# Kernel tuning notes

Measured on AMD Instinct MI355X. Metric: run time of the kernel, lower is better.

Reference implementation:

```python
import jax, jax.numpy as jnp
import numpy as np
import math

N_QUBITS = 6
N_LAYERS = 3
OUT_DIM = 8
B = 131072
F = 24


def _gate_rx(a):
    # RX(a) = [[cos(a/2), -i sin(a/2)], [-i sin(a/2), cos(a/2)]]; a: scalar or [B]
    c = jnp.cos(a / 2).astype(jnp.complex64)
    s = (-1j * jnp.sin(a / 2)).astype(jnp.complex64)
    return jnp.stack([jnp.stack([c, s], -1), jnp.stack([s, c], -1)], -2)


def _gate_ry(a):
    c = jnp.cos(a / 2).astype(jnp.complex64)
    s = jnp.sin(a / 2).astype(jnp.complex64)
    return jnp.stack([jnp.stack([c, -s], -1), jnp.stack([s, c], -1)], -2)


def _gate_rz(a):
    # RZ(a) = diag(e^{-ia/2}, e^{ia/2})
    e = jnp.exp(-0.5j * a.astype(jnp.complex64))
    z = jnp.zeros_like(e)
    return jnp.stack([jnp.stack([e, z], -1), jnp.stack([z, jnp.conj(e)], -1)], -2)


def _apply_1q(state, gate, q, batched):
    # state: [B] + [2]*N_QUBITS ; gate: [2,2] or [B,2,2]
    s = jnp.moveaxis(state, 1 + q, 1)
    if batched:
        out = jnp.einsum('bij,bj...->bi...', gate, s)
    else:
        out = jnp.einsum('ij,bj...->bi...', gate, s)
    return jnp.moveaxis(out, 1, 1 + q)


def _apply_cnot(state, c, t):
    # flip target where control bit == 1
    cax = 1 + c
    s0 = jnp.take(state, 0, axis=cax)
    s1 = jnp.take(state, 1, axis=cax)
    tax = 1 + t if t < c else t  # control axis removed
    s1 = jnp.flip(s1, axis=tax)
    return jnp.stack([s0, s1], axis=cax)


def _circuit(x, theta):
    Bn = x.shape[0]
    # pooling branch of forward: chunks of size ceil(F/n_qubits)=4, mean each
    x_packed = x.reshape(Bn, N_QUBITS, F // N_QUBITS).mean(-1)
    angles = jnp.clip(x_packed, -6.0, 6.0) / 6.0 * math.pi  # [B, n_qubits]

    state = jnp.zeros((Bn,) + (2,) * N_QUBITS, dtype=jnp.complex64)
    state = state.at[(slice(None),) + (0,) * N_QUBITS].set(1.0)

    # angle encoding: RX(a_q), RZ(0.5*a_q) per qubit (batched gates)
    for q in range(N_QUBITS):
        state = _apply_1q(state, _gate_rx(angles[:, q]), q, batched=True)
        state = _apply_1q(state, _gate_rz(0.5 * angles[:, q]), q, batched=True)

    for l in range(N_LAYERS):
        for q in range(N_QUBITS - 1):
            state = _apply_cnot(state, q, q + 1)
        state = _apply_cnot(state, N_QUBITS - 1, 0)
        for q in range(N_QUBITS):
            state = _apply_1q(state, _gate_rx(theta[l, q, 0]), q, batched=False)
            state = _apply_1q(state, _gate_ry(theta[l, q, 1]), q, batched=False)
            state = _apply_1q(state, _gate_rz(theta[l, q, 2]), q, batched=False)

    probs = jnp.abs(state) ** 2  # real
    meas = []
    for k in range(OUT_DIM):
        q = k % N_QUBITS
        if k % 2 == 0:  # PauliZ
            pq = jnp.sum(probs, axis=tuple(a for a in range(1, N_QUBITS + 1) if a != 1 + q))
            meas.append(pq[:, 0] - pq[:, 1])
        else:  # PauliX: Re <psi| X_q |psi>
            flipped = jnp.flip(state, axis=1 + q)
            meas.append(jnp.real(jnp.sum(jnp.conj(state) * flipped, axis=tuple(range(1, N_QUBITS + 1)))))
    return jnp.stack(meas, axis=1).astype(jnp.float32)  # [B, out_dim]


def setup_inputs() -> dict:
    key = jax.random.key(0)
    k1, k2 = jax.random.split(key)
    x = jax.random.normal(k1, (B, F), dtype=jnp.float32)
    theta = jax.random.normal(k2, (N_LAYERS, N_QUBITS, 3), dtype=jnp.float32) * 0.1
    return {"x": x, "theta": theta}


def reference(x, theta):
    return _circuit(x, theta)
```

## Files before the change

### kernel.cpp

```cpp
#include <hip/hip_runtime.h>
#include <math.h>


struct cf { float r, i; };

__device__ __forceinline__ cf cmul(cf a, cf b) {
    return { fmaf(a.r, b.r, -a.i * b.i), fmaf(a.r, b.i, a.i * b.r) };
}
__device__ __forceinline__ cf cmac(cf acc, cf g, cf v) {
    acc.r = fmaf(g.r, v.r, fmaf(-g.i, v.i, acc.r));
    acc.i = fmaf(g.r, v.i, fmaf(g.i, v.r, acc.i));
    return acc;
}

template<int M>
__device__ __forceinline__ void apply1q(cf* st, cf g00, cf g01, cf g10, cf g11) {
#pragma unroll
    for (int i = 0; i < 64; ++i) {
        if (i & M) continue;
        cf a = st[i], b = st[i + M];
        cf na = cmul(g00, a); na = cmac(na, g01, b);
        cf nb = cmul(g10, a); nb = cmac(nb, g11, b);
        st[i] = na; st[i + M] = nb;
    }
}

template<int MC, int MT>
__device__ __forceinline__ void cnot(cf* st) {
#pragma unroll
    for (int i = 0; i < 64; ++i) {
        if ((i & MC) && !(i & MT)) {
            cf tmp = st[i]; st[i] = st[i + MT]; st[i + MT] = tmp;
        }
    }
}

__global__ __launch_bounds__(256, 2) void qsim_kernel(
    const float* __restrict__ x, const float* __restrict__ theta,
    float* __restrict__ out) {
    __shared__ float gs[18 * 8];
    const int t = threadIdx.x;
    if (t < 18) {
        const float* th = theta + t * 3;
        float sx, cx, sy, cy, sz, cz;
        __sincosf(0.5f * th[0], &sx, &cx);
        __sincosf(0.5f * th[1], &sy, &cy);
        __sincosf(0.5f * th[2], &sz, &cz);
        cf m00 = {  cy * cx,  sy * sx };
        cf m01 = { -sy * cx, -cy * sx };
        cf m10 = {  sy * cx, -cy * sx };
        cf m11 = {  cy * cx, -sy * sx };
        cf e0 = { cz, -sz }, e1 = { cz, sz };
        cf g00 = cmul(e0, m00), g01 = cmul(e0, m01);
        cf g10 = cmul(e1, m10), g11 = cmul(e1, m11);
        float* o = gs + t * 8;
        o[0] = g00.r; o[1] = g00.i; o[2] = g01.r; o[3] = g01.i;
        o[4] = g10.r; o[5] = g10.i; o[6] = g11.r; o[7] = g11.i;
    }
    __syncthreads();

    const int b = blockIdx.x * 256 + t;

    const float4* xv = reinterpret_cast<const float4*>(x + (size_t)b * 24);
    cf v0[6], v1[6];
#pragma unroll
    for (int q = 0; q < 6; ++q) {
        float4 xq = xv[q];
        float m = (xq.x + xq.y + xq.z + xq.w) * 0.25f;
        m = fminf(fmaxf(m, -6.0f), 6.0f);
        float a = m * 0.52359877559829887308f;
        float s2, c2, s4, c4;
        __sincosf(0.50f * a, &s2, &c2);
        __sincosf(0.25f * a, &s4, &c4);
        v0[q] = { c4 * c2, -s4 * c2 };
        v1[q] = { s4 * s2, -c4 * s2 };
    }

    cf st[64];
    st[0] = v0[0]; st[32] = v1[0];
#pragma unroll
    for (int q = 1; q < 6; ++q) {
        const int m = 32 >> q;
#pragma unroll
        for (int i = 0; i < 64; i += 2 * m) {
            st[i + m] = cmul(st[i], v1[q]);
            st[i]     = cmul(st[i], v0[q]);
        }
    }

#pragma unroll
    for (int l = 0; l < 3; ++l) {
        cnot<32, 16>(st);
        cnot<16,  8>(st);
        cnot< 8,  4>(st);
        cnot< 4,  2>(st);
        cnot< 2,  1>(st);
        cnot< 1, 32>(st);
        const float* g = gs + l * 48;
#define G4(o) cf{g[(o)+0], g[(o)+1]}, cf{g[(o)+2], g[(o)+3]}, \
              cf{g[(o)+4], g[(o)+5]}, cf{g[(o)+6], g[(o)+7]}
        apply1q<32>(st, G4(0));
        apply1q<16>(st, G4(8));
        apply1q< 8>(st, G4(16));
        apply1q< 4>(st, G4(24));
        apply1q< 2>(st, G4(32));
        apply1q< 1>(st, G4(40));
#undef G4
    }

    float s[8] = {0, 0, 0, 0, 0, 0, 0, 0};
#pragma unroll
    for (int i = 0; i < 64; ++i) {
        float p = fmaf(st[i].r, st[i].r, st[i].i * st[i].i);
        const int gi = (((i >> 5) & 1) << 2) | (((i >> 3) & 1) << 1) | ((i >> 1) & 1);
        s[gi] += p;
    }
    float z0 = (s[0] + s[1] + s[2] + s[3]) - (s[4] + s[5] + s[6] + s[7]);
    float z2 = (s[0] + s[1] + s[4] + s[5]) - (s[2] + s[3] + s[6] + s[7]);
    float z4 = (s[0] + s[2] + s[4] + s[6]) - (s[1] + s[3] + s[5] + s[7]);

    float x1 = 0.0f, x3 = 0.0f, x5 = 0.0f;
#pragma unroll
    for (int i = 0; i < 64; ++i) {
        if (!(i & 16)) x1 = fmaf(st[i].r, st[i + 16].r, fmaf(st[i].i, st[i + 16].i, x1));
        if (!(i &  4)) x3 = fmaf(st[i].r, st[i +  4].r, fmaf(st[i].i, st[i +  4].i, x3));
        if (!(i &  1)) x5 = fmaf(st[i].r, st[i +  1].r, fmaf(st[i].i, st[i +  1].i, x5));
    }
    x1 *= 2.0f; x3 *= 2.0f; x5 *= 2.0f;

    float4* ov = reinterpret_cast<float4*>(out + (size_t)b * 8);
    ov[0] = make_float4(z0, x1, z2, x3);
    ov[1] = make_float4(z4, x5, z0, x1);
}

extern "C" void kernel_launch(void* const* d_in, const int* in_sizes, int n_in,
                              void* d_out, int out_size, void* d_ws, size_t ws_size,
                              hipStream_t stream) {
    const float* x     = (const float*)d_in[0];
    const float* theta = (const float*)d_in[1];
    float* out = (float*)d_out;
    const int B = in_sizes[0] / 24;
    qsim_kernel<<<dim3(B / 256), dim3(256), 0, stream>>>(x, theta, out);
}
```

Measured before the change: 88.52 us.

## Split each statevector across four lanes using DPP cross-lane exchanges

Each 64-amplitude state is now spread across four lanes with 16 amplitudes per lane, and the launch uses four times as many threads. The two high qubits become lane bits, so their gates, CNOTs and measurements use DPP lane shuffles and selects. Per-thread register use drops, which allows higher occupancy (launch bounds raised to 4 blocks). In exchange, every lane redundantly loads the input and computes its trig, shuffle instructions are added, and outputs become scattered scalar stores.

Result: no change. 89.97 us (+1.6%).

```diff
diff --git a/kernel.cpp b/kernel.cpp
--- a/kernel.cpp
+++ b/kernel.cpp
@@ -13,10 +13,21 @@
     return acc;
 }
 
+constexpr int DPP_X1  = 0xB1;
+constexpr int DPP_X2  = 0x4E;
+constexpr int DPP_C01 = 0xB4;
+
+template<int CTRL>
+__device__ __forceinline__ float dppf(float v) {
+    return __int_as_float(__builtin_amdgcn_mov_dpp(__float_as_int(v), CTRL, 0xF, 0xF, true));
+}
+template<int CTRL>
+__device__ __forceinline__ cf dppc(cf v) { return { dppf<CTRL>(v.r), dppf<CTRL>(v.i) }; }
+
 template<int M>
 __device__ __forceinline__ void apply1q(cf* st, cf g00, cf g01, cf g10, cf g11) {
 #pragma unroll
-    for (int i = 0; i < 64; ++i) {
+    for (int i = 0; i < 16; ++i) {
         if (i & M) continue;
         cf a = st[i], b = st[i + M];
         cf na = cmul(g00, a); na = cmac(na, g01, b);
@@ -25,17 +36,29 @@
     }
 }
 
-template<int MC, int MT>
-__device__ __forceinline__ void cnot(cf* st) {
+template<int XCTRL>
+__device__ __forceinline__ void apply1q_lane(cf* st, bool hi, cf g00, cf g01, cf g10, cf g11) {
+    cf ga, gb;
+    ga.r = hi ? g11.r : g00.r;  ga.i = hi ? g11.i : g00.i;
+    gb.r = hi ? g10.r : g01.r;  gb.i = hi ? g10.i : g01.i;
 #pragma unroll
-    for (int i = 0; i < 64; ++i) {
-        if ((i & MC) && !(i & MT)) {
-            cf tmp = st[i]; st[i] = st[i + MT]; st[i + MT] = tmp;
-        }
+    for (int i = 0; i < 16; ++i) {
+        cf part = dppc<XCTRL>(st[i]);
+        cf n = cmul(ga, st[i]);
+        n = cmac(n, gb, part);
+        st[i] = n;
     }
 }
 
-__global__ __launch_bounds__(256, 2) void qsim_kernel(
+template<int MC, int MT>
+__device__ __forceinline__ void cnot_local(cf* st) {
+#pragma unroll
+    for (int i = 0; i < 16; ++i) {
+        if ((i & MC) && !(i & MT)) { cf t = st[i]; st[i] = st[i + MT]; st[i + MT] = t; }
+    }
+}
+
+__global__ __launch_bounds__(256, 4) void qsim_kernel(
     const float* __restrict__ x, const float* __restrict__ theta,
     float* __restrict__ out) {
     __shared__ float gs[18 * 8];
@@ -59,9 +82,13 @@
     }
     __syncthreads();
 
-    const int b = blockIdx.x * 256 + t;
+    const int g = blockIdx.x * 256 + t;
+    const int e = g >> 2;
+    const int p = g & 3;
+    const bool l1 = (p & 2) != 0;
+    const bool l0 = (p & 1) != 0;
 
-    const float4* xv = reinterpret_cast<const float4*>(x + (size_t)b * 24);
+    const float4* xv = reinterpret_cast<const float4*>(x + (size_t)e * 24);
     cf v0[6], v1[6];
 #pragma unroll
     for (int q = 0; q < 6; ++q) {
@@ -76,61 +103,79 @@
         v1[q] = { s4 * s2, -c4 * s2 };
     }
 
-    cf st[64];
-    st[0] = v0[0]; st[32] = v1[0];
+    cf f0, f1;
+    f0.r = l1 ? v1[0].r : v0[0].r;  f0.i = l1 ? v1[0].i : v0[0].i;
+    f1.r = l0 ? v1[1].r : v0[1].r;  f1.i = l0 ? v1[1].i : v0[1].i;
+
+    cf st[16];
+    st[0] = cmul(f0, f1);
 #pragma unroll
-    for (int q = 1; q < 6; ++q) {
-        const int m = 32 >> q;
+    for (int q = 2; q < 6; ++q) {
+        const int m = 8 >> (q - 2);
 #pragma unroll
-        for (int i = 0; i < 64; i += 2 * m) {
+        for (int i = 0; i < 16; i += 2 * m) {
             st[i + m] = cmul(st[i], v1[q]);
             st[i]     = cmul(st[i], v0[q]);
         }
     }
 
+#pragma unroll 1
+    for (int l = 0; l < 3; ++l) {
 #pragma unroll
-    for (int l = 0; l < 3; ++l) {
-        cnot<32, 16>(st);
-        cnot<16,  8>(st);
-        cnot< 8,  4>(st);
-        cnot< 4,  2>(st);
-        cnot< 2,  1>(st);
-        cnot< 1, 32>(st);
-        const float* g = gs + l * 48;
-#define G4(o) cf{g[(o)+0], g[(o)+1]}, cf{g[(o)+2], g[(o)+3]}, \
-              cf{g[(o)+4], g[(o)+5]}, cf{g[(o)+6], g[(o)+7]}
-        apply1q<32>(st, G4(0));
-        apply1q<16>(st, G4(8));
-        apply1q< 8>(st, G4(16));
-        apply1q< 4>(st, G4(24));
-        apply1q< 2>(st, G4(32));
-        apply1q< 1>(st, G4(40));
+        for (int i = 0; i < 16; ++i) st[i] = dppc<DPP_C01>(st[i]);
+#pragma unroll
+        for (int i = 0; i < 8; ++i) {
+            cf lo = st[i], hi = st[i + 8];
+            st[i].r     = l0 ? hi.r : lo.r;  st[i].i     = l0 ? hi.i : lo.i;
+            st[i + 8].r = l0 ? lo.r : hi.r;  st[i + 8].i = l0 ? lo.i : hi.i;
+        }
+        cnot_local<8, 4>(st);
+        cnot_local<4, 2>(st);
+        cnot_local<2, 1>(st);
+#pragma unroll
+        for (int i = 1; i < 16; i += 2) st[i] = dppc<DPP_X2>(st[i]);
+
+        const float* gg = gs + l * 48;
+#define G4(k) cf{gg[8*(k)+0], gg[8*(k)+1]}, cf{gg[8*(k)+2], gg[8*(k)+3]}, \
+              cf{gg[8*(k)+4], gg[8*(k)+5]}, cf{gg[8*(k)+6], gg[8*(k)+7]}
+        apply1q_lane<DPP_X2>(st, l1, G4(0));
+        apply1q_lane<DPP_X1>(st, l0, G4(1));
+        apply1q<8>(st, G4(2));
+        apply1q<4>(st, G4(3));
+        apply1q<2>(st, G4(4));
+        apply1q<1>(st, G4(5));
 #undef G4
     }
 
-    float s[8] = {0, 0, 0, 0, 0, 0, 0, 0};
+    float z0 = 0.f, z2 = 0.f, z4 = 0.f, x1s = 0.f, x3s = 0.f, x5s = 0.f;
 #pragma unroll
-    for (int i = 0; i < 64; ++i) {
-        float p = fmaf(st[i].r, st[i].r, st[i].i * st[i].i);
-        const int gi = (((i >> 5) & 1) << 2) | (((i >> 3) & 1) << 1) | ((i >> 1) & 1);
-        s[gi] += p;
+    for (int i = 0; i < 16; ++i) {
+        float pr = fmaf(st[i].r, st[i].r, st[i].i * st[i].i);
+        z0 += pr;
+        z2 = (i & 8) ? z2 - pr : z2 + pr;
+        z4 = (i & 2) ? z4 - pr : z4 + pr;
+        cf part = dppc<DPP_X1>(st[i]);
+        x1s = fmaf(st[i].r, part.r, fmaf(st[i].i, part.i, x1s));
     }
-    float z0 = (s[0] + s[1] + s[2] + s[3]) - (s[4] + s[5] + s[6] + s[7]);
-    float z2 = (s[0] + s[1] + s[4] + s[5]) - (s[2] + s[3] + s[6] + s[7]);
-    float z4 = (s[0] + s[2] + s[4] + s[6]) - (s[1] + s[3] + s[5] + s[7]);
+    if (l1) z0 = -z0;
+#pragma unroll
+    for (int i = 0; i < 16; ++i) {
+        if (!(i & 4)) x3s = fmaf(st[i].r, st[i + 4].r, fmaf(st[i].i, st[i + 4].i, x3s));
+        if (!(i & 1)) x5s = fmaf(st[i].r, st[i + 1].r, fmaf(st[i].i, st[i + 1].i, x5s));
+    }
+    x3s *= 2.f; x5s *= 2.f;
 
-    float x1 = 0.0f, x3 = 0.0f, x5 = 0.0f;
-#pragma unroll
-    for (int i = 0; i < 64; ++i) {
-        if (!(i & 16)) x1 = fmaf(st[i].r, st[i + 16].r, fmaf(st[i].i, st[i + 16].i, x1));
-        if (!(i &  4)) x3 = fmaf(st[i].r, st[i +  4].r, fmaf(st[i].i, st[i +  4].i, x3));
-        if (!(i &  1)) x5 = fmaf(st[i].r, st[i +  1].r, fmaf(st[i].i, st[i +  1].i, x5));
-    }
-    x1 *= 2.0f; x3 *= 2.0f; x5 *= 2.0f;
+    z0  += dppf<DPP_X1>(z0);   z0  += dppf<DPP_X2>(z0);
+    z2  += dppf<DPP_X1>(z2);   z2  += dppf<DPP_X2>(z2);
+    z4  += dppf<DPP_X1>(z4);   z4  += dppf<DPP_X2>(z4);
+    x1s += dppf<DPP_X1>(x1s);  x1s += dppf<DPP_X2>(x1s);
+    x3s += dppf<DPP_X1>(x3s);  x3s += dppf<DPP_X2>(x3s);
+    x5s += dppf<DPP_X1>(x5s);  x5s += dppf<DPP_X2>(x5s);
 
-    float4* ov = reinterpret_cast<float4*>(out + (size_t)b * 8);
-    ov[0] = make_float4(z0, x1, z2, x3);
-    ov[1] = make_float4(z4, x5, z0, x1);
+    float o0 = l1 ? (l0 ? x3s : z2) : (l0 ? x1s : z0);
+    float o1 = l1 ? (l0 ? x1s : z0) : (l0 ? x5s : z4);
+    out[(size_t)e * 8 + p] = o0;
+    out[(size_t)e * 8 + 4 + p] = o1;
 }
 
 extern "C" void kernel_launch(void* const* d_in, const int* in_sizes, int n_in,
@@ -140,5 +185,6 @@
     const float* theta = (const float*)d_in[1];
     float* out = (float*)d_out;
     const int B = in_sizes[0] / 24;
-    qsim_kernel<<<dim3(B / 256), dim3(256), 0, stream>>>(x, theta, out);
+    const int threads = B * 4;
+    qsim_kernel<<<dim3(threads / 256), dim3(256), 0, stream>>>(x, theta, out);
 }
```
